# Optimization experiments

Hardware: AMD Instinct MI355X
Metric: run time of the kernel (lower is better)

## Reference

```python
import jax, jax.numpy as jnp
import numpy as np

B, S, E, H = 2, 2048, 1024, 16
HD = E // H  # head_dim = 64


def setup_inputs() -> dict:
    key = jax.random.key(0)
    k1, k2, k3, k4, k5 = jax.random.split(key, 5)
    return {
        "hidden_states": jax.random.normal(k1, (B, S, E), dtype=jnp.float32),
        "w_attn": jax.random.normal(k2, (E, 3 * E), dtype=jnp.float32) * 0.02,
        "b_attn": jax.random.normal(k3, (3 * E,), dtype=jnp.float32) * 0.02,
        "w_proj": jax.random.normal(k4, (E, E), dtype=jnp.float32) * 0.02,
        "b_proj": jax.random.normal(k5, (E,), dtype=jnp.float32) * 0.02,
    }


def reference(hidden_states, w_attn, b_attn, w_proj, b_proj):
    b, s, e = hidden_states.shape
    # QKV projection (HF Conv1D: x @ W + b)
    qkv = hidden_states @ w_attn + b_attn  # [B,S,3E]
    q, k, v = jnp.split(qkv, 3, axis=-1)
    # [B,S,E] -> [B,H,S,HD]
    def split_heads(x):
        return x.reshape(b, s, H, HD).transpose(0, 2, 1, 3)
    q, k, v = split_heads(q), split_heads(k), split_heads(v)
    scale = 1.0 / float(HD) ** 0.5  # scale_attn_weights
    scores = jnp.einsum("bhqd,bhkd->bhqk", q, k) * scale  # [B,H,S,S]
    causal = jnp.tril(jnp.ones((s, s), dtype=bool))
    mask_value = jnp.finfo(scores.dtype).min
    scores = jnp.where(causal, scores, mask_value)
    attn = jax.nn.softmax(scores, axis=-1)
    # attn_dropout is identity (p=0.0)
    out = jnp.einsum("bhqk,bhkd->bhqd", attn, v)  # [B,H,S,HD]
    out = out.transpose(0, 2, 1, 3).reshape(b, s, e)  # merge heads
    out = out @ w_proj + b_proj  # c_proj; resid_dropout identity
    return out
```

## Files before the change

### kernel.cpp

```cpp
#include <hip/hip_runtime.h>
#include <hip/hip_bf16.h>

#define B_   2
#define S_   2048
#define E_   1024
#define H_   16
#define HD_  64
#define E3_  3072
#define M_   4096
#define QKS  2048
#define QSC  0.1803368801111f

using short8 = __attribute__((ext_vector_type(8))) short;
using f32x4  = __attribute__((ext_vector_type(4))) float;

__device__ __forceinline__ unsigned short f2bf(float f) {
  union { float f; unsigned v; } t; t.f = f;
  unsigned r = t.v + 0x7FFFu + ((t.v >> 16) & 1u);
  return (unsigned short)(r >> 16);
}

__device__ __forceinline__ float exp2_fast(float x) {
  float r;
  asm("v_exp_f32 %0, %1" : "=v"(r) : "v"(x));
  return r;
}

__device__ __forceinline__ void gload16(const void* g, void* l) {
  __builtin_amdgcn_global_load_lds(
      (const __attribute__((address_space(1))) unsigned int*)g,
      (__attribute__((address_space(3))) unsigned int*)l, 16, 0, 0);
}

__global__ void cvt_f32_bf16(const float* __restrict__ in,
                             unsigned short* __restrict__ out, int n) {
  int i = (blockIdx.x * blockDim.x + threadIdx.x) * 4;
  if (i < n) {
    float4 v = *(const float4*)(in + i);
    ushort4 o;
    o.x = f2bf(v.x); o.y = f2bf(v.y); o.z = f2bf(v.z); o.w = f2bf(v.w);
    *(ushort4*)(out + i) = o;
  }
}

__global__ void transpose_bf16(const float* __restrict__ W,
                               unsigned short* __restrict__ WT, int K, int N) {
  __shared__ float tile[32][33];
  int bn = blockIdx.x * 32, bk = blockIdx.y * 32;
  int tx = threadIdx.x & 31, ty = threadIdx.x >> 5;
  #pragma unroll
  for (int i = 0; i < 32; i += 8)
    tile[ty + i][tx] = W[(size_t)(bk + ty + i) * N + bn + tx];
  __syncthreads();
  #pragma unroll
  for (int i = 0; i < 32; i += 8)
    WT[(size_t)(bn + ty + i) * K + bk + tx] = f2bf(tile[tx][ty + i]);
}

template <int MODE>
__global__ __launch_bounds__(256) void gemm_bt_bias(
    const unsigned short* __restrict__ A,
    const unsigned short* __restrict__ BT,
    const float* __restrict__ bias,
    float* __restrict__ Cf,
    unsigned short* __restrict__ Cbf,
    unsigned short* __restrict__ Vt,
    int M, int N, int K) {
  __shared__ __align__(16) unsigned short As[128 * 64];
  __shared__ __align__(16) unsigned short Bs[128 * 64];
  const int t = threadIdx.x;
  const int lane = t & 63, w = t >> 6;
  const int wr = w >> 1, wc = w & 1;
  const int m0 = blockIdx.y * 128, n0 = blockIdx.x * 128;
  const int lrow = lane & 15, lkg = lane >> 4;
  const int srow = t >> 3;
  const int sc8  = (t & 7) * 8;
  const int sgc  = sc8 ^ (((t >> 3) & 7) << 3);

  f32x4 acc[4][4];
  const f32x4 z = {0.f, 0.f, 0.f, 0.f};
  #pragma unroll
  for (int i = 0; i < 4; ++i)
    #pragma unroll
    for (int j = 0; j < 4; ++j) acc[i][j] = z;

  for (int k0 = 0; k0 < K; k0 += 64) {
    __syncthreads();
    #pragma unroll
    for (int p = 0; p < 4; ++p) {
      const int r = srow + 32 * p;
      gload16(A  + (size_t)(m0 + r) * K + k0 + sgc, &As[r * 64 + sc8]);
      gload16(BT + (size_t)(n0 + r) * K + k0 + sgc, &Bs[r * 64 + sc8]);
    }
    __syncthreads();

    short8 af[4][2], bf[4][2];
    #pragma unroll
    for (int m = 0; m < 4; ++m) {
      const int row = wr * 64 + m * 16 + lrow;
      const int base = row * 64, sw = (row & 7) << 3;
      af[m][0] = *(const short8*)&As[base + ((lkg * 8) ^ sw)];
      af[m][1] = *(const short8*)&As[base + ((32 + lkg * 8) ^ sw)];
    }
    #pragma unroll
    for (int n = 0; n < 4; ++n) {
      const int row = wc * 64 + n * 16 + lrow;
      const int base = row * 64, sw = (row & 7) << 3;
      bf[n][0] = *(const short8*)&Bs[base + ((lkg * 8) ^ sw)];
      bf[n][1] = *(const short8*)&Bs[base + ((32 + lkg * 8) ^ sw)];
    }
    #pragma unroll
    for (int m = 0; m < 4; ++m)
      #pragma unroll
      for (int n = 0; n < 4; ++n) {
        acc[m][n] = __builtin_amdgcn_mfma_f32_16x16x32_bf16(af[m][0], bf[n][0],
                                                            acc[m][n], 0, 0, 0);
        acc[m][n] = __builtin_amdgcn_mfma_f32_16x16x32_bf16(af[m][1], bf[n][1],
                                                            acc[m][n], 0, 0, 0);
      }
  }

  const int r0 = (lane >> 4) * 4, c0 = lane & 15;
  #pragma unroll
  for (int m = 0; m < 4; ++m) {
    #pragma unroll
    for (int n = 0; n < 4; ++n) {
      const int row = m0 + wr * 64 + m * 16 + r0;
      const int col = n0 + wc * 64 + n * 16 + c0;
      const float bv = bias[col];
      if (MODE == 0) {
        #pragma unroll
        for (int r = 0; r < 4; ++r)
          Cf[(size_t)(row + r) * N + col] = acc[m][n][r] + bv;
      } else {
        if (col < 2 * E_) {
          const float sc = (col < E_) ? QSC : 1.0f;
          #pragma unroll
          for (int r = 0; r < 4; ++r)
            Cbf[(size_t)(row + r) * QKS + col] = f2bf((acc[m][n][r] + bv) * sc);
        } else {
          const int hd = col - 2 * E_;
          ushort4 o;
          o.x = f2bf(acc[m][n][0] + bv);
          o.y = f2bf(acc[m][n][1] + bv);
          o.z = f2bf(acc[m][n][2] + bv);
          o.w = f2bf(acc[m][n][3] + bv);
          *(ushort4*)&Vt[(((size_t)(row >> 11) * H_ + (hd >> 6)) * HD_ +
                          (hd & 63)) * (size_t)S_ + (row & 2047)] = o;
        }
      }
    }
  }
}

__global__ __launch_bounds__(256) void flash_attn(
    const unsigned short* __restrict__ qk,
    const unsigned short* __restrict__ Vt,
    unsigned short* __restrict__ aout) {
  __shared__ __align__(16) unsigned short Ks[2][64 * 64];
  __shared__ __align__(16) unsigned short Vs[2][64 * 64];
  __shared__ __align__(16) unsigned short Ps[4][16 * 64];

  const int t = threadIdx.x, lane = t & 63, w = t >> 6;
  const int bh = blockIdx.x;
  const int yy = blockIdx.y;
  const int pi = yy & 7, pv = yy >> 3;
  int qt;
  switch (pv) {
    case 0:  qt = pi;      break;
    case 1:  qt = 15 - pi; break;
    case 2:  qt = 16 + pi; break;
    default: qt = 31 - pi; break;
  }
  const int b = bh >> 4, h = bh & 15;
  const int lq = lane & 15;
  const int g  = lane >> 4;
  const int lk8 = g * 8;
  const int swzq = (lq & 7) << 3;
  const size_t basebs = (size_t)b * S_;
  const f32x4 z = {0.f, 0.f, 0.f, 0.f};

  short8 qf[2];
  {
    const int qrow = qt * 64 + w * 16 + lq;
    const unsigned short* qp = qk + (basebs + qrow) * QKS + h * HD_;
    qf[0] = *(const short8*)(qp + lk8);
    qf[1] = *(const short8*)(qp + 32 + lk8);
  }

  float l_q = 0.f;
  f32x4 o_acc[4];
  #pragma unroll
  for (int n = 0; n < 4; ++n) o_acc[n] = z;

  const int sr = t >> 3, scc = (t & 7) * 8;
  const unsigned short* kp0 =
      qk + (basebs + sr) * QKS + E_ + h * HD_ + (scc ^ ((sr & 7) << 3));
  const unsigned short* kp1 = kp0 + 32 * QKS;
  const unsigned short* vp0 =
      Vt + ((size_t)bh * HD_ + sr) * S_ + (scc ^ ((sr & 7) << 3));
  const unsigned short* vp1 = vp0 + 32 * S_;

  auto stage = [&](int buf, int kt) {
    const size_t koff = (size_t)kt * 64 * QKS;
    const size_t voff = (size_t)kt * 64;
    gload16(kp0 + koff, &Ks[buf][t * 8]);
    gload16(kp1 + koff, &Ks[buf][t * 8 + 2048]);
    gload16(vp0 + voff, &Vs[buf][t * 8]);
    gload16(vp1 + voff, &Vs[buf][t * 8 + 2048]);
  };

  stage(0, 0);
  __syncthreads();
  int cur = 0;

  for (int kt = 0; kt <= qt; ++kt) {
    if (kt < qt) stage(cur ^ 1, kt + 1);

    f32x4 st[4];
    __builtin_amdgcn_s_setprio(1);
    #pragma unroll
    for (int f = 0; f < 4; ++f) {
      const int rowb = (f * 16 + lq) * 64;
      short8 kf0 = *(const short8*)&Ks[cur][rowb + (lk8 ^ swzq)];
      short8 kf1 = *(const short8*)&Ks[cur][rowb + ((lk8 + 32) ^ swzq)];
      st[f] = __builtin_amdgcn_mfma_f32_16x16x32_bf16(kf0, qf[0], z, 0, 0, 0);
      st[f] = __builtin_amdgcn_mfma_f32_16x16x32_bf16(kf1, qf[1], st[f], 0, 0, 0);
    }
    __builtin_amdgcn_s_setprio(0);

    if (kt == qt) {
      const int qcol = w * 16 + lq;
      #pragma unroll
      for (int f = 0; f < 4; ++f)
        #pragma unroll
        for (int r = 0; r < 4; ++r)
          if (16 * f + 4 * g + r > qcol) st[f][r] = -1e30f;
    }

    unsigned pw[4][2];
    #pragma unroll
    for (int f = 0; f < 4; ++f) {
      float p0 = exp2_fast(st[f][0]);
      float p1 = exp2_fast(st[f][1]);
      float p2 = exp2_fast(st[f][2]);
      float p3 = exp2_fast(st[f][3]);
      l_q += (p0 + p1) + (p2 + p3);
      asm("v_cvt_pk_bf16_f32 %0, %1, %2" : "=v"(pw[f][0]) : "v"(p0), "v"(p1));
      asm("v_cvt_pk_bf16_f32 %0, %1, %2" : "=v"(pw[f][1]) : "v"(p2), "v"(p3));
    }

    {
      unsigned short* pr = &Ps[w][lq * 64];
      #pragma unroll
      for (int f = 0; f < 4; ++f) {
        *(unsigned*)&pr[(16 * f + 4 * g) ^ swzq]       = pw[f][0];
        *(unsigned*)&pr[((16 * f + 4 * g + 2) ^ swzq)] = pw[f][1];
      }
    }

    short8 pa0 = *(const short8*)&Ps[w][lq * 64 + (lk8 ^ swzq)];
    short8 pa1 = *(const short8*)&Ps[w][lq * 64 + ((lk8 + 32) ^ swzq)];
    __builtin_amdgcn_s_setprio(1);
    #pragma unroll
    for (int n = 0; n < 4; ++n) {
      const int rowb = (n * 16 + lq) * 64;
      short8 vb0 = *(const short8*)&Vs[cur][rowb + (lk8 ^ swzq)];
      short8 vb1 = *(const short8*)&Vs[cur][rowb + ((lk8 + 32) ^ swzq)];
      o_acc[n] = __builtin_amdgcn_mfma_f32_16x16x32_bf16(pa0, vb0, o_acc[n], 0, 0, 0);
      o_acc[n] = __builtin_amdgcn_mfma_f32_16x16x32_bf16(pa1, vb1, o_acc[n], 0, 0, 0);
    }
    __builtin_amdgcn_s_setprio(0);

    __syncthreads();
    cur ^= 1;
  }

  l_q += __shfl_xor(l_q, 16);
  l_q += __shfl_xor(l_q, 32);
  const int qbase = qt * 64 + w * 16 + 4 * g;
  #pragma unroll
  for (int r = 0; r < 4; ++r) {
    const float lr = __shfl(l_q, 4 * g + r);
    const float inv = 1.0f / lr;
    const int row = qbase + r;
    #pragma unroll
    for (int n = 0; n < 4; ++n)
      aout[(basebs + row) * E_ + h * HD_ + n * 16 + lq] =
          f2bf(o_acc[n][r] * inv);
  }
}

extern "C" void kernel_launch(void* const* d_in, const int* in_sizes, int n_in,
                              void* d_out, int out_size, void* d_ws, size_t ws_size,
                              hipStream_t stream) {
  const float* X  = (const float*)d_in[0];
  const float* Wa = (const float*)d_in[1];
  const float* ba = (const float*)d_in[2];
  const float* Wp = (const float*)d_in[3];
  const float* bp = (const float*)d_in[4];
  float* out = (float*)d_out;

  char* ws = (char*)d_ws;
  unsigned short* Xb  = (unsigned short*)ws; ws += (size_t)M_ * E_ * 2;
  unsigned short* WaT = (unsigned short*)ws; ws += (size_t)E3_ * E_ * 2;
  unsigned short* WpT = (unsigned short*)ws; ws += (size_t)E_ * E_ * 2;
  unsigned short* QK  = (unsigned short*)ws; ws += (size_t)M_ * QKS * 2;
  unsigned short* Vt  = (unsigned short*)ws; ws += (size_t)M_ * E_ * 2;
  unsigned short* AO  = (unsigned short*)ws; ws += (size_t)M_ * E_ * 2;

  cvt_f32_bf16<<<(M_ * E_ / 4 + 255) / 256, 256, 0, stream>>>(X, Xb, M_ * E_);
  transpose_bf16<<<dim3(E3_ / 32, E_ / 32), 256, 0, stream>>>(Wa, WaT, E_, E3_);
  transpose_bf16<<<dim3(E_ / 32, E_ / 32), 256, 0, stream>>>(Wp, WpT, E_, E_);
  gemm_bt_bias<1><<<dim3(E3_ / 128, M_ / 128), 256, 0, stream>>>(
      Xb, WaT, ba, nullptr, QK, Vt, M_, E3_, E_);
  flash_attn<<<dim3(B_ * H_, S_ / 64), 256, 0, stream>>>(QK, Vt, AO);
  gemm_bt_bias<0><<<dim3(E_ / 128, M_ / 128), 256, 0, stream>>>(
      AO, WpT, bp, out, nullptr, nullptr, M_, E_, E_);
}
```

Before: 111.3 us.

## Process 128 query rows per attention block to reuse each staged K/V tile

Each flash-attention workgroup now handles two 64-row query chunks (128 rows) instead of one. Each K/V tile staged in shared memory is used by both chunks, which halves global K/V traffic per query and halves the number of barriers per query row. The query-tile ordering is simplified to a pairing of short and long tiles. The trade-offs are half as many workgroups (512 instead of 1024), more registers per thread for the doubled accumulators, and a coarser causal load imbalance.

```diff
diff --git a/kernel.cpp b/kernel.cpp
--- a/kernel.cpp
+++ b/kernel.cpp
@@ -164,14 +164,7 @@
   const int t = threadIdx.x, lane = t & 63, w = t >> 6;
   const int bh = blockIdx.x;
   const int yy = blockIdx.y;
-  const int pi = yy & 7, pv = yy >> 3;
-  int qt;
-  switch (pv) {
-    case 0:  qt = pi;      break;
-    case 1:  qt = 15 - pi; break;
-    case 2:  qt = 16 + pi; break;
-    default: qt = 31 - pi; break;
-  }
+  const int qt = (yy < 8) ? yy : 23 - yy;
   const int b = bh >> 4, h = bh & 15;
   const int lq = lane & 15;
   const int g  = lane >> 4;
@@ -179,19 +172,23 @@
   const int swzq = (lq & 7) << 3;
   const size_t basebs = (size_t)b * S_;
   const f32x4 z = {0.f, 0.f, 0.f, 0.f};
-
-  short8 qf[2];
-  {
-    const int qrow = qt * 64 + w * 16 + lq;
+  const int qbase = qt * 128;
+
+  short8 qf[2][2];
+  #pragma unroll
+  for (int c = 0; c < 2; ++c) {
+    const int qrow = qbase + c * 64 + w * 16 + lq;
     const unsigned short* qp = qk + (basebs + qrow) * QKS + h * HD_;
-    qf[0] = *(const short8*)(qp + lk8);
-    qf[1] = *(const short8*)(qp + 32 + lk8);
-  }
-
-  float l_q = 0.f;
-  f32x4 o_acc[4];
-  #pragma unroll
-  for (int n = 0; n < 4; ++n) o_acc[n] = z;
+    qf[c][0] = *(const short8*)(qp + lk8);
+    qf[c][1] = *(const short8*)(qp + 32 + lk8);
+  }
+
+  float l_c[2] = {0.f, 0.f};
+  f32x4 o_acc[2][4];
+  #pragma unroll
+  for (int c = 0; c < 2; ++c)
+    #pragma unroll
+    for (int n = 0; n < 4; ++n) o_acc[c][n] = z;
 
   const int sr = t >> 3, scc = (t & 7) * 8;
   const unsigned short* kp0 =
@@ -210,84 +207,98 @@
     gload16(vp1 + voff, &Vs[buf][t * 8 + 2048]);
   };
 
+  const int nkt = 2 * qt + 2;
   stage(0, 0);
   __syncthreads();
   int cur = 0;
 
-  for (int kt = 0; kt <= qt; ++kt) {
-    if (kt < qt) stage(cur ^ 1, kt + 1);
-
-    f32x4 st[4];
-    __builtin_amdgcn_s_setprio(1);
-    #pragma unroll
-    for (int f = 0; f < 4; ++f) {
-      const int rowb = (f * 16 + lq) * 64;
-      short8 kf0 = *(const short8*)&Ks[cur][rowb + (lk8 ^ swzq)];
-      short8 kf1 = *(const short8*)&Ks[cur][rowb + ((lk8 + 32) ^ swzq)];
-      st[f] = __builtin_amdgcn_mfma_f32_16x16x32_bf16(kf0, qf[0], z, 0, 0, 0);
-      st[f] = __builtin_amdgcn_mfma_f32_16x16x32_bf16(kf1, qf[1], st[f], 0, 0, 0);
-    }
-    __builtin_amdgcn_s_setprio(0);
-
-    if (kt == qt) {
-      const int qcol = w * 16 + lq;
-      #pragma unroll
-      for (int f = 0; f < 4; ++f)
+  for (int kt = 0; kt < nkt; ++kt) {
+    if (kt + 1 < nkt) stage(cur ^ 1, kt + 1);
+    const bool diag = (kt >= 2 * qt);
+
+    #pragma unroll
+    for (int c = 0; c < 2; ++c) {
+      if (diag && kt == 2 * qt + 1 && c == 0) continue;
+
+      f32x4 st[4];
+      __builtin_amdgcn_s_setprio(1);
+      #pragma unroll
+      for (int f = 0; f < 4; ++f) {
+        const int rowb = (f * 16 + lq) * 64;
+        short8 kf0 = *(const short8*)&Ks[cur][rowb + (lk8 ^ swzq)];
+        short8 kf1 = *(const short8*)&Ks[cur][rowb + ((lk8 + 32) ^ swzq)];
+        st[f] = __builtin_amdgcn_mfma_f32_16x16x32_bf16(kf0, qf[c][0], z, 0, 0, 0);
+        st[f] = __builtin_amdgcn_mfma_f32_16x16x32_bf16(kf1, qf[c][1], st[f], 0, 0, 0);
+      }
+      __builtin_amdgcn_s_setprio(0);
+
+      if (diag) {
+        const int qcol = c * 64 + w * 16 + lq;
+        const int kbase = (kt - 2 * qt) * 64;
         #pragma unroll
-        for (int r = 0; r < 4; ++r)
-          if (16 * f + 4 * g + r > qcol) st[f][r] = -1e30f;
-    }
-
-    unsigned pw[4][2];
-    #pragma unroll
-    for (int f = 0; f < 4; ++f) {
-      float p0 = exp2_fast(st[f][0]);
-      float p1 = exp2_fast(st[f][1]);
-      float p2 = exp2_fast(st[f][2]);
-      float p3 = exp2_fast(st[f][3]);
-      l_q += (p0 + p1) + (p2 + p3);
-      asm("v_cvt_pk_bf16_f32 %0, %1, %2" : "=v"(pw[f][0]) : "v"(p0), "v"(p1));
-      asm("v_cvt_pk_bf16_f32 %0, %1, %2" : "=v"(pw[f][1]) : "v"(p2), "v"(p3));
-    }
-
-    {
-      unsigned short* pr = &Ps[w][lq * 64];
+        for (int f = 0; f < 4; ++f)
+          #pragma unroll
+          for (int r = 0; r < 4; ++r)
+            if (kbase + 16 * f + 4 * g + r > qcol) st[f][r] = -1e30f;
+      }
+
+      unsigned pw[4][2];
       #pragma unroll
       for (int f = 0; f < 4; ++f) {
-        *(unsigned*)&pr[(16 * f + 4 * g) ^ swzq]       = pw[f][0];
-        *(unsigned*)&pr[((16 * f + 4 * g + 2) ^ swzq)] = pw[f][1];
-      }
-    }
-
-    short8 pa0 = *(const short8*)&Ps[w][lq * 64 + (lk8 ^ swzq)];
-    short8 pa1 = *(const short8*)&Ps[w][lq * 64 + ((lk8 + 32) ^ swzq)];
-    __builtin_amdgcn_s_setprio(1);
-    #pragma unroll
-    for (int n = 0; n < 4; ++n) {
-      const int rowb = (n * 16 + lq) * 64;
-      short8 vb0 = *(const short8*)&Vs[cur][rowb + (lk8 ^ swzq)];
-      short8 vb1 = *(const short8*)&Vs[cur][rowb + ((lk8 + 32) ^ swzq)];
-      o_acc[n] = __builtin_amdgcn_mfma_f32_16x16x32_bf16(pa0, vb0, o_acc[n], 0, 0, 0);
-      o_acc[n] = __builtin_amdgcn_mfma_f32_16x16x32_bf16(pa1, vb1, o_acc[n], 0, 0, 0);
-    }
-    __builtin_amdgcn_s_setprio(0);
+        float p0 = exp2_fast(st[f][0]);
+        float p1 = exp2_fast(st[f][1]);
+        float p2 = exp2_fast(st[f][2]);
+        float p3 = exp2_fast(st[f][3]);
+        l_c[c] += (p0 + p1) + (p2 + p3);
+        asm("v_cvt_pk_bf16_f32 %0, %1, %2" : "=v"(pw[f][0]) : "v"(p0), "v"(p1));
+        asm("v_cvt_pk_bf16_f32 %0, %1, %2" : "=v"(pw[f][1]) : "v"(p2), "v"(p3));
+      }
+
+      {
+        unsigned short* pr = &Ps[w][lq * 64];
+        #pragma unroll
+        for (int f = 0; f < 4; ++f) {
+          *(unsigned*)&pr[(16 * f + 4 * g) ^ swzq]       = pw[f][0];
+          *(unsigned*)&pr[((16 * f + 4 * g + 2) ^ swzq)] = pw[f][1];
+        }
+      }
+
+      short8 pa0 = *(const short8*)&Ps[w][lq * 64 + (lk8 ^ swzq)];
+      short8 pa1 = *(const short8*)&Ps[w][lq * 64 + ((lk8 + 32) ^ swzq)];
+      __builtin_amdgcn_s_setprio(1);
+      #pragma unroll
+      for (int n = 0; n < 4; ++n) {
+        const int rowb = (n * 16 + lq) * 64;
+        short8 vb0 = *(const short8*)&Vs[cur][rowb + (lk8 ^ swzq)];
+        short8 vb1 = *(const short8*)&Vs[cur][rowb + ((lk8 + 32) ^ swzq)];
+        o_acc[c][n] = __builtin_amdgcn_mfma_f32_16x16x32_bf16(pa0, vb0,
+                                                              o_acc[c][n], 0, 0, 0);
+        o_acc[c][n] = __builtin_amdgcn_mfma_f32_16x16x32_bf16(pa1, vb1,
+                                                              o_acc[c][n], 0, 0, 0);
+      }
+      __builtin_amdgcn_s_setprio(0);
+    }
 
     __syncthreads();
     cur ^= 1;
   }
 
-  l_q += __shfl_xor(l_q, 16);
-  l_q += __shfl_xor(l_q, 32);
-  const int qbase = qt * 64 + w * 16 + 4 * g;
-  #pragma unroll
-  for (int r = 0; r < 4; ++r) {
-    const float lr = __shfl(l_q, 4 * g + r);
-    const float inv = 1.0f / lr;
-    const int row = qbase + r;
-    #pragma unroll
-    for (int n = 0; n < 4; ++n)
-      aout[(basebs + row) * E_ + h * HD_ + n * 16 + lq] =
-          f2bf(o_acc[n][r] * inv);
+  #pragma unroll
+  for (int c = 0; c < 2; ++c) {
+    float l_q = l_c[c];
+    l_q += __shfl_xor(l_q, 16);
+    l_q += __shfl_xor(l_q, 32);
+    const int rb = qbase + c * 64 + w * 16 + 4 * g;
+    #pragma unroll
+    for (int r = 0; r < 4; ++r) {
+      const float lr = __shfl(l_q, 4 * g + r);
+      const float inv = 1.0f / lr;
+      const int row = rb + r;
+      #pragma unroll
+      for (int n = 0; n < 4; ++n)
+        aout[(basebs + row) * E_ + h * HD_ + n * 16 + lq] =
+            f2bf(o_acc[c][n][r] * inv);
+    }
   }
 }
 
@@ -314,7 +325,7 @@
   transpose_bf16<<<dim3(E_ / 32, E_ / 32), 256, 0, stream>>>(Wp, WpT, E_, E_);
   gemm_bt_bias<1><<<dim3(E3_ / 128, M_ / 128), 256, 0, stream>>>(
       Xb, WaT, ba, nullptr, QK, Vt, M_, E3_, E_);
-  flash_attn<<<dim3(B_ * H_, S_ / 64), 256, 0, stream>>>(QK, Vt, AO);
+  flash_attn<<<dim3(B_ * H_, S_ / 128), 256, 0, stream>>>(QK, Vt, AO);
   gemm_bt_bias<0><<<dim3(E_ / 128, M_ / 128), 256, 0, stream>>>(
       AO, WpT, bp, out, nullptr, nullptr, M_, E_, E_);
 }
```

Result: slower. 125.4 us (+12.7%).

## Split KV range of longest causal query tiles and merge partials in combine kernel

Applied to the files above, without the earlier changes.

The eight longest causal query tiles per head (qt 24..31) now run as two blocks each, every block covering half of the key range. Partial unnormalised outputs and row sums go to fp32 workspace, and a new combine kernel adds them, normalises and writes bf16. The grid order is remapped so the heaviest work is scheduled first. The goal is to shorten the critical path of the imbalanced causal grid. It costs an extra kernel launch and extra fp32 global traffic, and summing partials directly relies on the softmax using a fixed max reference.

```diff
diff --git a/kernel.cpp b/kernel.cpp
--- a/kernel.cpp
+++ b/kernel.cpp
@@ -156,7 +156,9 @@
 __global__ __launch_bounds__(256) void flash_attn(
     const unsigned short* __restrict__ qk,
     const unsigned short* __restrict__ Vt,
-    unsigned short* __restrict__ aout) {
+    unsigned short* __restrict__ aout,
+    float* __restrict__ Opart,
+    float* __restrict__ Lpart) {
   __shared__ __align__(16) unsigned short Ks[2][64 * 64];
   __shared__ __align__(16) unsigned short Vs[2][64 * 64];
   __shared__ __align__(16) unsigned short Ps[4][16 * 64];
@@ -164,13 +166,18 @@
   const int t = threadIdx.x, lane = t & 63, w = t >> 6;
   const int bh = blockIdx.x;
   const int yy = blockIdx.y;
-  const int pi = yy & 7, pv = yy >> 3;
-  int qt;
-  switch (pv) {
-    case 0:  qt = pi;      break;
-    case 1:  qt = 15 - pi; break;
-    case 2:  qt = 16 + pi; break;
-    default: qt = 31 - pi; break;
+  int qt, lo, hi, part = 0;
+  bool split = false;
+  if (yy < 8) {
+    qt = 23 - yy; lo = 0; hi = qt + 1;
+  } else if (yy < 24) {
+    const int idx = yy - 8;
+    qt = 31 - (idx >> 1); part = idx & 1;
+    const int mid = (qt + 2) >> 1;
+    lo = part ? mid : 0; hi = part ? qt + 1 : mid;
+    split = true;
+  } else {
+    qt = 39 - yy; lo = 0; hi = qt + 1;
   }
   const int b = bh >> 4, h = bh & 15;
   const int lq = lane & 15;
@@ -210,12 +217,12 @@
     gload16(vp1 + voff, &Vs[buf][t * 8 + 2048]);
   };
 
-  stage(0, 0);
+  stage(0, lo);
   __syncthreads();
   int cur = 0;
 
-  for (int kt = 0; kt <= qt; ++kt) {
-    if (kt < qt) stage(cur ^ 1, kt + 1);
+  for (int kt = lo; kt < hi; ++kt) {
+    if (kt + 1 < hi) stage(cur ^ 1, kt + 1);
 
     f32x4 st[4];
     __builtin_amdgcn_s_setprio(1);
@@ -278,17 +285,52 @@
 
   l_q += __shfl_xor(l_q, 16);
   l_q += __shfl_xor(l_q, 32);
-  const int qbase = qt * 64 + w * 16 + 4 * g;
-  #pragma unroll
-  for (int r = 0; r < 4; ++r) {
-    const float lr = __shfl(l_q, 4 * g + r);
-    const float inv = 1.0f / lr;
-    const int row = qbase + r;
-    #pragma unroll
-    for (int n = 0; n < 4; ++n)
-      aout[(basebs + row) * E_ + h * HD_ + n * 16 + lq] =
-          f2bf(o_acc[n][r] * inv);
-  }
+
+  if (!split) {
+    const int qbase = qt * 64 + w * 16 + 4 * g;
+    #pragma unroll
+    for (int r = 0; r < 4; ++r) {
+      const float lr = __shfl(l_q, 4 * g + r);
+      const float inv = 1.0f / lr;
+      const int row = qbase + r;
+      #pragma unroll
+      for (int n = 0; n < 4; ++n)
+        aout[(basebs + row) * E_ + h * HD_ + n * 16 + lq] =
+            f2bf(o_acc[n][r] * inv);
+    }
+  } else {
+    const int sidx = (bh << 3) | (qt - 24);
+    float* Ob = Opart + ((size_t)(sidx * 2 + part) << 12);
+    #pragma unroll
+    for (int r = 0; r < 4; ++r) {
+      const int qrow = w * 16 + 4 * g + r;
+      #pragma unroll
+      for (int n = 0; n < 4; ++n)
+        Ob[qrow * 64 + n * 16 + lq] = o_acc[n][r];
+    }
+    if (g == 0)
+      Lpart[(sidx * 2 + part) * 64 + w * 16 + lq] = l_q;
+  }
+}
+
+__global__ __launch_bounds__(256) void attn_combine(
+    const float* __restrict__ Opart, const float* __restrict__ Lpart,
+    unsigned short* __restrict__ aout) {
+  const int s = blockIdx.x;
+  const int bh = s >> 3, qt = 24 + (s & 7);
+  const int b = bh >> 4, h = bh & 15;
+  const int t = threadIdx.x;
+  const int q = t >> 2;
+  const int d0 = (t & 3) * 16;
+  const float l = Lpart[(s * 2 + 0) * 64 + q] + Lpart[(s * 2 + 1) * 64 + q];
+  const float inv = 1.0f / l;
+  const float* p0 = Opart + ((size_t)(s * 2 + 0) << 12) + q * 64 + d0;
+  const float* p1 = Opart + ((size_t)(s * 2 + 1) << 12) + q * 64 + d0;
+  unsigned short* dst =
+      aout + ((size_t)b * S_ + qt * 64 + q) * E_ + h * HD_ + d0;
+  #pragma unroll
+  for (int i = 0; i < 16; ++i)
+    dst[i] = f2bf((p0[i] + p1[i]) * inv);
 }
 
 extern "C" void kernel_launch(void* const* d_in, const int* in_sizes, int n_in,
@@ -308,13 +350,16 @@
   unsigned short* QK  = (unsigned short*)ws; ws += (size_t)M_ * QKS * 2;
   unsigned short* Vt  = (unsigned short*)ws; ws += (size_t)M_ * E_ * 2;
   unsigned short* AO  = (unsigned short*)ws; ws += (size_t)M_ * E_ * 2;
+  float* Opart = (float*)ws; ws += (size_t)256 * 2 * 64 * 64 * 4;
+  float* Lpart = (float*)ws; ws += (size_t)256 * 2 * 64 * 4;
 
   cvt_f32_bf16<<<(M_ * E_ / 4 + 255) / 256, 256, 0, stream>>>(X, Xb, M_ * E_);
   transpose_bf16<<<dim3(E3_ / 32, E_ / 32), 256, 0, stream>>>(Wa, WaT, E_, E3_);
   transpose_bf16<<<dim3(E_ / 32, E_ / 32), 256, 0, stream>>>(Wp, WpT, E_, E_);
   gemm_bt_bias<1><<<dim3(E3_ / 128, M_ / 128), 256, 0, stream>>>(
       Xb, WaT, ba, nullptr, QK, Vt, M_, E3_, E_);
-  flash_attn<<<dim3(B_ * H_, S_ / 64), 256, 0, stream>>>(QK, Vt, AO);
+  flash_attn<<<dim3(B_ * H_, 40), 256, 0, stream>>>(QK, Vt, AO, Opart, Lpart);
+  attn_combine<<<256, 256, 0, stream>>>(Opart, Lpart, AO);
   gemm_bt_bias<0><<<dim3(E_ / 128, M_ / 128), 256, 0, stream>>>(
       AO, WpT, bp, out, nullptr, nullptr, M_, E_, E_);
 }
```

Measured after the change: 112.1 us. No clear change (+0.8%).
